# Performance work log

Hardware: AMD Instinct MI355X
Metric: run time of the kernel (lower is better)

The kernel has to match this reference:

```python
import jax, jax.numpy as jnp
import numpy as np

TOKENS, D_IN, D_OUT, R = 8192, 4096, 4096, 16
SCALE = 2.0

def setup_inputs() -> dict:
    key = jax.random.key(0)
    ks = jax.random.split(key, 5)
    return {
        "x": jax.random.normal(ks[0], (TOKENS, D_IN), dtype=jnp.float32),
        "weight": jax.random.normal(ks[1], (D_OUT, D_IN), dtype=jnp.float32) * 0.02,
        "bias": jax.random.normal(ks[2], (D_OUT,), dtype=jnp.float32) * 0.01,
        "lora_A": jax.random.normal(ks[3], (R, D_IN), dtype=jnp.float32) * 0.02,
        "lora_B": jax.random.normal(ks[4], (D_OUT, R), dtype=jnp.float32) * 0.02,
    }

def reference(x, weight, bias, lora_A, lora_B):
    # y = x W^T + bias + scale * x (B A)^T
    # Reassociate to avoid materializing the [D_OUT, D_IN] B@A matrix:
    # x (B A)^T = (x A^T) B^T  -- same math, low-rank path.
    base = jnp.einsum('ti,oi->to', x, weight) + bias          # [T, D_OUT]
    lora = jnp.einsum('tr,or->to', jnp.einsum('ti,ri->tr', x, lora_A), lora_B)
    return base + SCALE * lora
```

## Files before the change

kernel.cpp:

```cpp
#include <hip/hip_runtime.h>
#include <hip/hip_bf16.h>
#include <stdint.h>

#define TOKENS 8192
#define DIN 4096
#define DOUT 4096
#define RNK 16
#define LORA_SCALE 2.0f

typedef __attribute__((ext_vector_type(8))) __bf16 bf16x8;
typedef __attribute__((ext_vector_type(4))) float f32x4;

__device__ __forceinline__ unsigned short f2bf(float f) {
    union { float f; unsigned int u; } v; v.f = f;
    unsigned int u = v.u;
    unsigned int r = (u + 0x7fffu + ((u >> 16) & 1u)) >> 16;
    return (unsigned short)r;
}

__device__ __forceinline__ void async_copy16(const void* g, void* l) {
    __builtin_amdgcn_global_load_lds(
        (const __attribute__((address_space(1))) void*)g,
        (__attribute__((address_space(3))) void*)l,
        16, 0, 0);
}

__global__ void cast_x_kernel(const float4* __restrict__ x, ushort4* __restrict__ xb) {
    int i = blockIdx.x * blockDim.x + threadIdx.x;
    float4 v = x[i];
    ushort4 o;
    o.x = f2bf(v.x); o.y = f2bf(v.y); o.z = f2bf(v.z); o.w = f2bf(v.w);
    xb[i] = o;
}

__global__ void fold_w_kernel(const float* __restrict__ W,
                              const float* __restrict__ lA,
                              const float* __restrict__ lB,
                              ushort* __restrict__ Wb) {
    int o  = blockIdx.y;
    int i0 = (blockIdx.x * blockDim.x + threadIdx.x) * 4;
    __shared__ float sB[RNK];
    if (threadIdx.x < RNK) sB[threadIdx.x] = lB[(size_t)o * RNK + threadIdx.x];
    __syncthreads();
    float4 w = *(const float4*)(W + (size_t)o * DIN + i0);
    float ax = 0.f, ay = 0.f, az = 0.f, aw = 0.f;
#pragma unroll
    for (int r = 0; r < RNK; r++) {
        float4 a = *(const float4*)(lA + (size_t)r * DIN + i0);
        float b = sB[r];
        ax += b * a.x; ay += b * a.y; az += b * a.z; aw += b * a.w;
    }
    ushort4 outv;
    outv.x = f2bf(w.x + LORA_SCALE * ax);
    outv.y = f2bf(w.y + LORA_SCALE * ay);
    outv.z = f2bf(w.z + LORA_SCALE * az);
    outv.w = f2bf(w.w + LORA_SCALE * aw);
    *(ushort4*)(Wb + (size_t)o * DIN + i0) = outv;
}

#define BM 128
#define BN 128
#define BK 64

__global__ __launch_bounds__(256) void gemm_bias_kernel(
    const ushort* __restrict__ Xb, const ushort* __restrict__ Wb,
    const float* __restrict__ bias, float* __restrict__ Y) {
    const int N = DOUT, K = DIN;
    __shared__ ushort sA[BM * BK];
    __shared__ ushort sB[BN * BK];

    const int tid  = threadIdx.x;
    const int lane = tid & 63;
    const int wave = tid >> 6;
    const int m0 = blockIdx.y * BM;
    const int n0 = blockIdx.x * BN;

    const int wm64 = (wave & 1) * 64;
    const int wn64 = (wave >> 1) * 64;

    const int srow = tid >> 3;
    const int p    = tid & 7;
    const int scol = (p ^ (srow & 7)) * 8;
    const ushort* gA = Xb + (size_t)(m0 + srow) * K + scol;
    const ushort* gB = Wb + (size_t)(n0 + srow) * K + scol;
    ushort* lAp = &sA[tid * 8];
    ushort* lBp = &sB[tid * 8];

    const int lr  = lane & 15;
    const int q   = lane >> 4;
    const int swc = lr & 7;
    const int c0  = ((0 * 4 + q) ^ swc) * 8;
    const int c1  = ((1 * 4 + q) ^ swc) * 8;

    f32x4 acc[4][4] = {};

    for (int k0 = 0; k0 < K; k0 += BK) {
        __syncthreads();
#pragma unroll
        for (int j = 0; j < 4; j++) {
            async_copy16(gA + (size_t)(j * 32) * K, lAp + j * 2048);
            async_copy16(gB + (size_t)(j * 32) * K, lBp + j * 2048);
        }
        gA += BK; gB += BK;
        __syncthreads();

#pragma unroll
        for (int s = 0; s < 2; s++) {
            const int cs = s ? c1 : c0;
            bf16x8 af[4], bfr[4];
#pragma unroll
            for (int t = 0; t < 4; t++) {
                af[t]  = *(const bf16x8*)(&sA[(wm64 + t * 16 + lr) * BK + cs]);
                bfr[t] = *(const bf16x8*)(&sB[(wn64 + t * 16 + lr) * BK + cs]);
            }
#pragma unroll
            for (int im = 0; im < 4; im++)
#pragma unroll
                for (int in = 0; in < 4; in++)
                    acc[im][in] = __builtin_amdgcn_mfma_f32_16x16x32_bf16(
                        af[im], bfr[in], acc[im][in], 0, 0, 0);
        }
    }

    const int col  = lane & 15;
    const int qrow = (lane >> 4) * 4;
#pragma unroll
    for (int in = 0; in < 4; in++) {
        const int n = n0 + wn64 + in * 16 + col;
        const float bv = bias[n];
#pragma unroll
        for (int im = 0; im < 4; im++) {
            const int m = m0 + wm64 + im * 16 + qrow;
            float* yp = Y + (size_t)m * N + n;
            yp[0 * (size_t)N] = acc[im][in].x + bv;
            yp[1 * (size_t)N] = acc[im][in].y + bv;
            yp[2 * (size_t)N] = acc[im][in].z + bv;
            yp[3 * (size_t)N] = acc[im][in].w + bv;
        }
    }
}

extern "C" void kernel_launch(void* const* d_in, const int* in_sizes, int n_in,
                              void* d_out, int out_size, void* d_ws, size_t ws_size,
                              hipStream_t stream) {
    const float* x    = (const float*)d_in[0];
    const float* W    = (const float*)d_in[1];
    const float* bias = (const float*)d_in[2];
    const float* lA   = (const float*)d_in[3];
    const float* lB   = (const float*)d_in[4];
    float* Y = (float*)d_out;

    ushort* xb = (ushort*)d_ws;
    ushort* wb = xb + (size_t)TOKENS * DIN;

    cast_x_kernel<<<(TOKENS * DIN / 4) / 256, 256, 0, stream>>>(
        (const float4*)x, (ushort4*)xb);
    fold_w_kernel<<<dim3(DIN / (256 * 4), DOUT), 256, 0, stream>>>(W, lA, lB, wb);
    gemm_bias_kernel<<<dim3(DOUT / BN, TOKENS / BM), 256, 0, stream>>>(xb, wb, bias, Y);
}
```

Measured before the change: 605.8 us.

## Rewrite GEMM with 256x256 tiles, 4-stage async LDS pipeline and XCD swizzle

The bf16 GEMM moves to 256x256 block tiles with 512 threads, where each wave computes a 128x64 sub-tile. It adds a four-slot LDS ring fed by async global-to-LDS copies with explicit vmcnt waits, so loads run ahead while the MFMAs execute. It also remaps block IDs so neighbouring tiles land on the same XCD for better L2 reuse, and raises MFMA wave priority. In exchange it needs more registers per thread (128 accumulator floats) and 128 KB of LDS per block, and the correctness of the hand-written barrier and waitcnt schedule is a risk.

```diff
diff --git a/kernel.cpp b/kernel.cpp
--- a/kernel.cpp
+++ b/kernel.cpp
@@ -58,86 +58,134 @@
     *(ushort4*)(Wb + (size_t)o * DIN + i0) = outv;
 }
 
-#define BM 128
-#define BN 128
-#define BK 64
-
-__global__ __launch_bounds__(256) void gemm_bias_kernel(
+#define BM 256
+#define BN 256
+#define BK 32
+#define NTILES (DIN / BK)
+#define SLOT_U16 16384
+#define SLOT_BYTES 32768
+#define B_OFF_BYTES 16384
+
+__global__ __launch_bounds__(512, 2) void gemm_bias_kernel(
     const ushort* __restrict__ Xb, const ushort* __restrict__ Wb,
     const float* __restrict__ bias, float* __restrict__ Y) {
-    const int N = DOUT, K = DIN;
-    __shared__ ushort sA[BM * BK];
-    __shared__ ushort sB[BN * BK];
+
+    __shared__ ushort smem[4 * SLOT_U16];
 
     const int tid  = threadIdx.x;
     const int lane = tid & 63;
     const int wave = tid >> 6;
-    const int m0 = blockIdx.y * BM;
-    const int n0 = blockIdx.x * BN;
-
-    const int wm64 = (wave & 1) * 64;
-    const int wn64 = (wave >> 1) * 64;
-
-    const int srow = tid >> 3;
-    const int p    = tid & 7;
-    const int scol = (p ^ (srow & 7)) * 8;
-    const ushort* gA = Xb + (size_t)(m0 + srow) * K + scol;
-    const ushort* gB = Wb + (size_t)(n0 + srow) * K + scol;
-    ushort* lAp = &sA[tid * 8];
-    ushort* lBp = &sB[tid * 8];
-
-    const int lr  = lane & 15;
-    const int q   = lane >> 4;
-    const int swc = lr & 7;
-    const int c0  = ((0 * 4 + q) ^ swc) * 8;
-    const int c1  = ((1 * 4 + q) ^ swc) * 8;
-
-    f32x4 acc[4][4] = {};
-
-    for (int k0 = 0; k0 < K; k0 += BK) {
-        __syncthreads();
-#pragma unroll
-        for (int j = 0; j < 4; j++) {
-            async_copy16(gA + (size_t)(j * 32) * K, lAp + j * 2048);
-            async_copy16(gB + (size_t)(j * 32) * K, lBp + j * 2048);
-        }
-        gA += BK; gB += BK;
-        __syncthreads();
-
-#pragma unroll
-        for (int s = 0; s < 2; s++) {
-            const int cs = s ? c1 : c0;
-            bf16x8 af[4], bfr[4];
-#pragma unroll
-            for (int t = 0; t < 4; t++) {
-                af[t]  = *(const bf16x8*)(&sA[(wm64 + t * 16 + lr) * BK + cs]);
-                bfr[t] = *(const bf16x8*)(&sB[(wn64 + t * 16 + lr) * BK + cs]);
-            }
-#pragma unroll
-            for (int im = 0; im < 4; im++)
-#pragma unroll
-                for (int in = 0; in < 4; in++)
-                    acc[im][in] = __builtin_amdgcn_mfma_f32_16x16x32_bf16(
-                        af[im], bfr[in], acc[im][in], 0, 0, 0);
+
+    const int bid  = blockIdx.x;
+    const int sbid = (bid & 7) * 64 + (bid >> 3);
+    const int m0 = (sbid >> 4) * BM;
+    const int n0 = (sbid & 15) * BN;
+
+    const int wm = (wave >> 2) * 128;
+    const int wn = (wave & 3) * 64;
+
+    auto srcoff = [](int ci) -> size_t {
+        const int L = ci >> 3, p = ci & 7;
+        const int u = p ^ (L & 7);
+        return (size_t)(2 * L + (u >> 2)) * DIN + (size_t)((u & 3) * 8);
+    };
+    const ushort* pA0 = Xb + (size_t)m0 * DIN + srcoff(tid);
+    const ushort* pA1 = Xb + (size_t)m0 * DIN + srcoff(tid + 512);
+    const ushort* pB0 = Wb + (size_t)n0 * DIN + srcoff(tid);
+    const ushort* pB1 = Wb + (size_t)n0 * DIN + srcoff(tid + 512);
+
+#define STAGE_A(slot) do { \
+        ushort* d_ = smem + (slot) * SLOT_U16 + tid * 8; \
+        async_copy16(pA0, d_); async_copy16(pA1, d_ + 4096); \
+        pA0 += BK; pA1 += BK; } while (0)
+#define STAGE_B(slot) do { \
+        ushort* d_ = smem + (slot) * SLOT_U16 + 8192 + tid * 8; \
+        async_copy16(pB0, d_); async_copy16(pB1, d_ + 4096); \
+        pB0 += BK; pB1 += BK; } while (0)
+
+    const int lr = lane & 15, qq = lane >> 4;
+    const int pp = (qq + 4 * (lr & 1)) ^ ((lr >> 1) & 7);
+    const int offA = ((wm >> 1) + (lr >> 1)) * 128 + pp * 16;
+    const int offB = ((wn >> 1) + (lr >> 1)) * 128 + pp * 16;
+    const char* smemc = (const char*)smem;
+
+    f32x4 acc[8][4] = {};
+    bf16x8 af[4], bfr[4];
+
+    STAGE_A(0); STAGE_B(0);
+    STAGE_A(1); STAGE_B(1);
+    STAGE_A(2); STAGE_B(2);
+    asm volatile("s_waitcnt vmcnt(8)" ::: "memory");
+    __builtin_amdgcn_s_barrier();
+
+#pragma unroll 1
+    for (int t = 0; t < NTILES; ++t) {
+        const char* sa = smemc + (size_t)(t & 3) * SLOT_BYTES;
+        const char* sb = sa + B_OFF_BYTES;
+        const int  stslot  = (t + 3) & 3;
+        const bool doStage = (t + 3 < NTILES);
+
+#pragma unroll
+        for (int f = 0; f < 4; f++) af[f]  = *(const bf16x8*)(sa + offA + f * 1024);
+#pragma unroll
+        for (int f = 0; f < 4; f++) bfr[f] = *(const bf16x8*)(sb + offB + f * 1024);
+        if (doStage) STAGE_A(stslot);
+        __builtin_amdgcn_s_barrier();
+        asm volatile("s_waitcnt lgkmcnt(0)" ::: "memory");
+        __builtin_amdgcn_s_setprio(1);
+#pragma unroll
+        for (int mf = 0; mf < 4; mf++)
+#pragma unroll
+            for (int nf = 0; nf < 4; nf++)
+                acc[mf][nf] = __builtin_amdgcn_mfma_f32_16x16x32_bf16(
+                    af[mf], bfr[nf], acc[mf][nf], 0, 0, 0);
+        __builtin_amdgcn_s_setprio(0);
+        __builtin_amdgcn_s_barrier();
+
+#pragma unroll
+        for (int f = 0; f < 4; f++) af[f] = *(const bf16x8*)(sa + offA + (4 + f) * 1024);
+        if (doStage) STAGE_B(stslot);
+        __builtin_amdgcn_s_barrier();
+        asm volatile("s_waitcnt lgkmcnt(0)" ::: "memory");
+        __builtin_amdgcn_s_setprio(1);
+#pragma unroll
+        for (int mf = 0; mf < 4; mf++)
+#pragma unroll
+            for (int nf = 0; nf < 4; nf++)
+                acc[4 + mf][nf] = __builtin_amdgcn_mfma_f32_16x16x32_bf16(
+                    af[mf], bfr[nf], acc[4 + mf][nf], 0, 0, 0);
+        __builtin_amdgcn_s_setprio(0);
+
+        if (t + 3 < NTILES) {
+            asm volatile("s_waitcnt vmcnt(8)" ::: "memory");
+            __builtin_amdgcn_s_barrier();
+        } else if (t + 3 == NTILES) {
+            asm volatile("s_waitcnt vmcnt(4)" ::: "memory");
+            __builtin_amdgcn_s_barrier();
+        } else if (t + 2 == NTILES) {
+            asm volatile("s_waitcnt vmcnt(0)" ::: "memory");
+            __builtin_amdgcn_s_barrier();
         }
     }
 
     const int col  = lane & 15;
     const int qrow = (lane >> 4) * 4;
 #pragma unroll
-    for (int in = 0; in < 4; in++) {
-        const int n = n0 + wn64 + in * 16 + col;
+    for (int nf = 0; nf < 4; nf++) {
+        const int n = n0 + wn + nf * 16 + col;
         const float bv = bias[n];
 #pragma unroll
-        for (int im = 0; im < 4; im++) {
-            const int m = m0 + wm64 + im * 16 + qrow;
-            float* yp = Y + (size_t)m * N + n;
-            yp[0 * (size_t)N] = acc[im][in].x + bv;
-            yp[1 * (size_t)N] = acc[im][in].y + bv;
-            yp[2 * (size_t)N] = acc[im][in].z + bv;
-            yp[3 * (size_t)N] = acc[im][in].w + bv;
+        for (int mf = 0; mf < 8; mf++) {
+            const int m = m0 + wm + mf * 16 + qrow;
+            float* yp = Y + (size_t)m * DOUT + n;
+            yp[0]                  = acc[mf][nf].x + bv;
+            yp[(size_t)DOUT]       = acc[mf][nf].y + bv;
+            yp[2 * (size_t)DOUT]   = acc[mf][nf].z + bv;
+            yp[3 * (size_t)DOUT]   = acc[mf][nf].w + bv;
         }
     }
+#undef STAGE_A
+#undef STAGE_B
 }
 
 extern "C" void kernel_launch(void* const* d_in, const int* in_sizes, int n_in,
@@ -156,5 +204,6 @@
     cast_x_kernel<<<(TOKENS * DIN / 4) / 256, 256, 0, stream>>>(
         (const float4*)x, (ushort4*)xb);
     fold_w_kernel<<<dim3(DIN / (256 * 4), DOUT), 256, 0, stream>>>(W, lA, lB, wb);
-    gemm_bias_kernel<<<dim3(DOUT / BN, TOKENS / BM), 256, 0, stream>>>(xb, wb, bias, Y);
-}
+    gemm_bias_kernel<<<dim3((TOKENS / BM) * (DOUT / BN)), 512, 0, stream>>>(
+        xb, wb, bias, Y);
+}
```

Measured after the change: 550.1 us. 9.2% less time.

## Rewrite GEMM with 256x256 tiles, double-buffered async LDS pipeline, and block swizzle

Applied to the files above, without the earlier changes.

Replaces the 128x128 single-buffered GEMM with a 256x256 tile run by 512 threads (8 waves, each computing 128x64). The K loop keeps two LDS stages in flight, issuing async global-to-LDS copies for tile t+2 while MFMAs run on the current tile, and interleaves barriers, lgkmcnt/vmcnt waits and setprio to overlap loads with compute. Block IDs are remapped across groups of 8 to improve L2 reuse. The aim is to hide global latency and cut per-FLOP LDS traffic. In exchange it uses 128KB of LDS per block and more registers per thread, so fewer blocks fit per CU, and the barrier protocol is fragile.

```diff
diff --git a/kernel.cpp b/kernel.cpp
--- a/kernel.cpp
+++ b/kernel.cpp
@@ -58,86 +58,150 @@
     *(ushort4*)(Wb + (size_t)o * DIN + i0) = outv;
 }
 
-#define BM 128
-#define BN 128
+#define BM 256
+#define BN 256
 #define BK 64
-
-__global__ __launch_bounds__(256) void gemm_bias_kernel(
+#define NT (DIN / BK)
+#define AREG 0
+#define BREG 32768
+
+__global__ __launch_bounds__(512, 2) void gemm_bias_kernel(
     const ushort* __restrict__ Xb, const ushort* __restrict__ Wb,
     const float* __restrict__ bias, float* __restrict__ Y) {
-    const int N = DOUT, K = DIN;
-    __shared__ ushort sA[BM * BK];
-    __shared__ ushort sB[BN * BK];
+
+    __shared__ ushort smem[65536];
 
     const int tid  = threadIdx.x;
     const int lane = tid & 63;
     const int wave = tid >> 6;
-    const int m0 = blockIdx.y * BM;
-    const int n0 = blockIdx.x * BN;
-
-    const int wm64 = (wave & 1) * 64;
-    const int wn64 = (wave >> 1) * 64;
-
-    const int srow = tid >> 3;
-    const int p    = tid & 7;
-    const int scol = (p ^ (srow & 7)) * 8;
-    const ushort* gA = Xb + (size_t)(m0 + srow) * K + scol;
-    const ushort* gB = Wb + (size_t)(n0 + srow) * K + scol;
-    ushort* lAp = &sA[tid * 8];
-    ushort* lBp = &sB[tid * 8];
-
-    const int lr  = lane & 15;
-    const int q   = lane >> 4;
-    const int swc = lr & 7;
-    const int c0  = ((0 * 4 + q) ^ swc) * 8;
-    const int c1  = ((1 * 4 + q) ^ swc) * 8;
-
-    f32x4 acc[4][4] = {};
-
-    for (int k0 = 0; k0 < K; k0 += BK) {
-        __syncthreads();
-#pragma unroll
-        for (int j = 0; j < 4; j++) {
-            async_copy16(gA + (size_t)(j * 32) * K, lAp + j * 2048);
-            async_copy16(gB + (size_t)(j * 32) * K, lBp + j * 2048);
-        }
-        gA += BK; gB += BK;
-        __syncthreads();
-
-#pragma unroll
-        for (int s = 0; s < 2; s++) {
-            const int cs = s ? c1 : c0;
-            bf16x8 af[4], bfr[4];
-#pragma unroll
-            for (int t = 0; t < 4; t++) {
-                af[t]  = *(const bf16x8*)(&sA[(wm64 + t * 16 + lr) * BK + cs]);
-                bfr[t] = *(const bf16x8*)(&sB[(wn64 + t * 16 + lr) * BK + cs]);
-            }
-#pragma unroll
-            for (int im = 0; im < 4; im++)
-#pragma unroll
-                for (int in = 0; in < 4; in++)
-                    acc[im][in] = __builtin_amdgcn_mfma_f32_16x16x32_bf16(
-                        af[im], bfr[in], acc[im][in], 0, 0, 0);
-        }
+
+    const int bid  = blockIdx.x;
+    const int sbid = (bid & 7) * 64 + (bid >> 3);
+    const int m0 = (sbid >> 4) * BM;
+    const int n0 = (sbid & 15) * BN;
+
+    const int wm128 = (wave >> 2) * 128;
+    const int wn64  = (wave & 3) * 64;
+    const int hA  = wave >> 2;
+    const int hB  = wn64 >> 7;
+    const int nB0 = wn64 & 127;
+
+    const int rowL = tid >> 3;
+    const int uu   = (tid & 7) ^ (rowL & 7);
+    const size_t prebase = (size_t)rowL * DIN + (size_t)(uu * 8);
+    const ushort* pA = Xb + (size_t)m0 * DIN + prebase;
+    const ushort* pB = Wb + (size_t)n0 * DIN + prebase;
+
+#define STAGE_H(reg, src, h, t) do { \
+        ushort* d_ = smem + (reg) + ((((t) & 1) << 1) + (h)) * 8192 + tid * 8; \
+        const ushort* s_ = (src) + (size_t)(h) * (128 * (size_t)DIN) + (size_t)(t) * 64; \
+        async_copy16(s_, d_); \
+        async_copy16(s_ + (size_t)64 * DIN, d_ + 4096); \
+    } while (0)
+
+    const int lr = lane & 15, qq = lane >> 4;
+    const int l0 = lr * 128 + ((qq ^ (lr & 7)) * 16);
+    const int l1 = lr * 128 + (((4 + qq) ^ (lr & 7)) * 16);
+    const char* smemc = (const char*)smem;
+    const char* aS0 = smemc + (0 + hA) * 16384;
+    const char* aS1 = smemc + (2 + hA) * 16384;
+    const char* bS0 = smemc + 65536 + (0 + hB) * 16384 + nB0 * 128;
+    const char* bS1 = smemc + 65536 + (2 + hB) * 16384 + nB0 * 128;
+
+#define LD8(p) (*(const bf16x8*)(p))
+#define BAR_LGKM do { \
+        __builtin_amdgcn_s_barrier(); \
+        asm volatile("s_waitcnt lgkmcnt(0)" ::: "memory"); \
+        __builtin_amdgcn_sched_barrier(0); \
+        __builtin_amdgcn_s_setprio(1); \
+    } while (0)
+#define CLOSE do { \
+        __builtin_amdgcn_s_setprio(0); \
+        __builtin_amdgcn_s_barrier(); \
+    } while (0)
+#define MFMA_Q(mo, no, A_, B_) do { \
+        _Pragma("unroll") \
+        for (int m_ = 0; m_ < 4; m_++) \
+        _Pragma("unroll") \
+        for (int n_ = 0; n_ < 2; n_++) \
+        _Pragma("unroll") \
+        for (int k_ = 0; k_ < 2; k_++) \
+            acc[(mo) + m_][(no) + n_] = __builtin_amdgcn_mfma_f32_16x16x32_bf16( \
+                A_[m_][k_], B_[n_][k_], acc[(mo) + m_][(no) + n_], 0, 0, 0); \
+    } while (0)
+
+    f32x4 acc[8][4] = {};
+    bf16x8 aa[4][2], b0[2][2], b1[2][2];
+
+    STAGE_H(AREG, pA, 0, 0); STAGE_H(AREG, pA, 1, 0);
+    STAGE_H(BREG, pB, 0, 0); STAGE_H(BREG, pB, 1, 0);
+    STAGE_H(AREG, pA, 0, 1); STAGE_H(AREG, pA, 1, 1);
+    STAGE_H(BREG, pB, 0, 1); STAGE_H(BREG, pB, 1, 1);
+    asm volatile("s_waitcnt vmcnt(8)" ::: "memory");
+    __builtin_amdgcn_s_barrier();
+
+#define KTILE(AS, BS, ts, doSt) do { \
+         \
+        _Pragma("unroll") \
+        for (int m_ = 0; m_ < 4; m_++) { \
+            aa[m_][0] = LD8(AS + m_ * 2048 + l0); \
+            aa[m_][1] = LD8(AS + m_ * 2048 + l1); } \
+        _Pragma("unroll") \
+        for (int n_ = 0; n_ < 2; n_++) { \
+            b0[n_][0] = LD8(BS + n_ * 2048 + l0); \
+            b0[n_][1] = LD8(BS + n_ * 2048 + l1); } \
+        BAR_LGKM; MFMA_Q(0, 0, aa, b0); CLOSE; \
+         \
+        _Pragma("unroll") \
+        for (int n_ = 0; n_ < 2; n_++) { \
+            b1[n_][0] = LD8(BS + (n_ + 2) * 2048 + l0); \
+            b1[n_][1] = LD8(BS + (n_ + 2) * 2048 + l1); } \
+        BAR_LGKM; MFMA_Q(0, 2, aa, b1); CLOSE; \
+         \
+        _Pragma("unroll") \
+        for (int m_ = 0; m_ < 4; m_++) { \
+            aa[m_][0] = LD8(AS + (m_ + 4) * 2048 + l0); \
+            aa[m_][1] = LD8(AS + (m_ + 4) * 2048 + l1); } \
+        if (doSt) { STAGE_H(BREG, pB, 0, ts); STAGE_H(BREG, pB, 1, ts); } \
+        BAR_LGKM; MFMA_Q(4, 2, aa, b1); CLOSE; \
+         \
+        if (doSt) { STAGE_H(AREG, pA, 0, ts); STAGE_H(AREG, pA, 1, ts); } \
+        BAR_LGKM; MFMA_Q(4, 0, aa, b0); \
+        __builtin_amdgcn_s_setprio(0); \
+        if (doSt) { asm volatile("s_waitcnt vmcnt(8)" ::: "memory"); } \
+        else      { asm volatile("s_waitcnt vmcnt(0)" ::: "memory"); } \
+        __builtin_amdgcn_s_barrier(); \
+    } while (0)
+
+#pragma unroll 1
+    for (int it = 0; it < NT / 2; ++it) {
+        const int t0 = 2 * it, t1 = 2 * it + 1;
+        KTILE(aS0, bS0, t0 + 2, (t0 + 2 < NT));
+        KTILE(aS1, bS1, t1 + 2, (t1 + 2 < NT));
     }
 
     const int col  = lane & 15;
     const int qrow = (lane >> 4) * 4;
 #pragma unroll
-    for (int in = 0; in < 4; in++) {
-        const int n = n0 + wn64 + in * 16 + col;
+    for (int nf = 0; nf < 4; nf++) {
+        const int n = n0 + wn64 + nf * 16 + col;
         const float bv = bias[n];
 #pragma unroll
-        for (int im = 0; im < 4; im++) {
-            const int m = m0 + wm64 + im * 16 + qrow;
-            float* yp = Y + (size_t)m * N + n;
-            yp[0 * (size_t)N] = acc[im][in].x + bv;
-            yp[1 * (size_t)N] = acc[im][in].y + bv;
-            yp[2 * (size_t)N] = acc[im][in].z + bv;
-            yp[3 * (size_t)N] = acc[im][in].w + bv;
+        for (int mf = 0; mf < 8; mf++) {
+            const int m = m0 + wm128 + mf * 16 + qrow;
+            float* yp = Y + (size_t)m * DOUT + n;
+            yp[0]                = acc[mf][nf].x + bv;
+            yp[(size_t)DOUT]     = acc[mf][nf].y + bv;
+            yp[2 * (size_t)DOUT] = acc[mf][nf].z + bv;
+            yp[3 * (size_t)DOUT] = acc[mf][nf].w + bv;
         }
     }
+#undef STAGE_H
+#undef KTILE
+#undef MFMA_Q
+#undef BAR_LGKM
+#undef CLOSE
+#undef LD8
 }
 
 extern "C" void kernel_launch(void* const* d_in, const int* in_sizes, int n_in,
@@ -156,5 +220,6 @@
     cast_x_kernel<<<(TOKENS * DIN / 4) / 256, 256, 0, stream>>>(
         (const float4*)x, (ushort4*)xb);
     fold_w_kernel<<<dim3(DIN / (256 * 4), DOUT), 256, 0, stream>>>(W, lA, lB, wb);
-    gemm_bias_kernel<<<dim3(DOUT / BN, TOKENS / BM), 256, 0, stream>>>(xb, wb, bias, Y);
-}
+    gemm_bias_kernel<<<dim3((TOKENS / BM) * (DOUT / BN)), 512, 0, stream>>>(
+        xb, wb, bias, Y);
+}
```

New measurement: 535.4 us. 1.13x faster.

## Triple-buffer GEMM with 256x128 tiles, BK=32 and swizzled block order

Applied to the files above, without the earlier changes.

Restructures the bf16 GEMM to a 256x128 block tile with BK=32 and a three-slot LDS ring. Asynchronous global-to-LDS copies for tile t+2 are issued while tile t is computed, with vmcnt waits replacing the double __syncthreads per iteration. Block IDs are remapped so that groups of blocks share rows or columns for L2 reuse, and launch bounds request 2 blocks per CU. The cast kernel is also turned into a grid-stride loop with a fixed grid. Each wave now holds 8x4 accumulators, which raises register pressure.

```diff
diff --git a/kernel.cpp b/kernel.cpp
--- a/kernel.cpp
+++ b/kernel.cpp
@@ -26,11 +26,14 @@
 }
 
 __global__ void cast_x_kernel(const float4* __restrict__ x, ushort4* __restrict__ xb) {
-    int i = blockIdx.x * blockDim.x + threadIdx.x;
-    float4 v = x[i];
-    ushort4 o;
-    o.x = f2bf(v.x); o.y = f2bf(v.y); o.z = f2bf(v.z); o.w = f2bf(v.w);
-    xb[i] = o;
+    const int total = TOKENS * DIN / 4;
+    for (int i = blockIdx.x * blockDim.x + threadIdx.x; i < total;
+         i += gridDim.x * blockDim.x) {
+        float4 v = x[i];
+        ushort4 o;
+        o.x = f2bf(v.x); o.y = f2bf(v.y); o.z = f2bf(v.z); o.w = f2bf(v.w);
+        xb[i] = o;
+    }
 }
 
 __global__ void fold_w_kernel(const float* __restrict__ W,
@@ -58,86 +61,111 @@
     *(ushort4*)(Wb + (size_t)o * DIN + i0) = outv;
 }
 
-#define BM 128
+#define BM 256
 #define BN 128
-#define BK 64
+#define BK 32
+#define NT (DIN / BK)
+#define SLOT_U16 12288
+#define SLOT_BYTES 24576
+#define B_OFF_BYTES 16384
 
-__global__ __launch_bounds__(256) void gemm_bias_kernel(
+__global__ __launch_bounds__(256, 2) void gemm_bias_kernel(
     const ushort* __restrict__ Xb, const ushort* __restrict__ Wb,
     const float* __restrict__ bias, float* __restrict__ Y) {
-    const int N = DOUT, K = DIN;
-    __shared__ ushort sA[BM * BK];
-    __shared__ ushort sB[BN * BK];
+
+    __shared__ ushort smem[3 * SLOT_U16];
 
     const int tid  = threadIdx.x;
     const int lane = tid & 63;
     const int wave = tid >> 6;
-    const int m0 = blockIdx.y * BM;
-    const int n0 = blockIdx.x * BN;
 
-    const int wm64 = (wave & 1) * 64;
-    const int wn64 = (wave >> 1) * 64;
+    const int bid  = blockIdx.x;
+    const int sbid = (bid & 7) * 128 + (bid >> 3);
+    const int m0 = (sbid >> 5) * BM;
+    const int n0 = (sbid & 31) * BN;
 
-    const int srow = tid >> 3;
-    const int p    = tid & 7;
-    const int scol = (p ^ (srow & 7)) * 8;
-    const ushort* gA = Xb + (size_t)(m0 + srow) * K + scol;
-    const ushort* gB = Wb + (size_t)(n0 + srow) * K + scol;
-    ushort* lAp = &sA[tid * 8];
-    ushort* lBp = &sB[tid * 8];
+    const int wm = (wave >> 1) * 128;
+    const int wn = (wave & 1) * 64;
 
-    const int lr  = lane & 15;
-    const int q   = lane >> 4;
-    const int swc = lr & 7;
-    const int c0  = ((0 * 4 + q) ^ swc) * 8;
-    const int c1  = ((1 * 4 + q) ^ swc) * 8;
+    const int rowS = tid >> 2;
+    const int gS   = (tid & 3) ^ ((rowS >> 1) & 3);
+    const ushort* pA = Xb + (size_t)(m0 + rowS) * DIN + gS * 8;
+    const ushort* pB = Wb + (size_t)(n0 + rowS) * DIN + gS * 8;
 
-    f32x4 acc[4][4] = {};
+#define STAGE(slot, t_) do { \
+        const size_t ko_ = (size_t)(t_) * BK; \
+        ushort* dA_ = smem + (slot) * SLOT_U16 + tid * 8; \
+        const ushort* sA_ = pA + ko_; \
+        async_copy16(sA_,                    dA_); \
+        async_copy16(sA_ +  64 * (size_t)DIN, dA_ + 2048); \
+        async_copy16(sA_ + 128 * (size_t)DIN, dA_ + 4096); \
+        async_copy16(sA_ + 192 * (size_t)DIN, dA_ + 6144); \
+        ushort* dB_ = smem + (slot) * SLOT_U16 + 8192 + tid * 8; \
+        const ushort* sB_ = pB + ko_; \
+        async_copy16(sB_,                    dB_); \
+        async_copy16(sB_ +  64 * (size_t)DIN, dB_ + 2048); \
+    } while (0)
 
-    for (int k0 = 0; k0 < K; k0 += BK) {
-        __syncthreads();
+    const int lr = lane & 15, q = lane >> 4;
+    const int gF = q ^ ((lr >> 1) & 3);
+    const int offA = (wm + lr) * 64 + gF * 16;
+    const int offB = B_OFF_BYTES + (wn + lr) * 64 + gF * 16;
+    const char* smemc = (const char*)smem;
+
+    f32x4 acc[8][4] = {};
+
+    STAGE(0, 0);
+    STAGE(1, 1);
+    asm volatile("s_waitcnt vmcnt(6)" ::: "memory");
+    __builtin_amdgcn_s_barrier();
+
+    int s = 0, s2 = 2;
+#pragma unroll 1
+    for (int t = 0; t < NT; ++t) {
+        if (t + 2 < NT) STAGE(s2, t + 2);
+
+        const char* base = smemc + s * SLOT_BYTES;
+        bf16x8 af[8], bf[4];
 #pragma unroll
-        for (int j = 0; j < 4; j++) {
-            async_copy16(gA + (size_t)(j * 32) * K, lAp + j * 2048);
-            async_copy16(gB + (size_t)(j * 32) * K, lBp + j * 2048);
-        }
-        gA += BK; gB += BK;
-        __syncthreads();
+        for (int m = 0; m < 8; m++) af[m] = *(const bf16x8*)(base + offA + 1024 * m);
+#pragma unroll
+        for (int n = 0; n < 4; n++) bf[n] = *(const bf16x8*)(base + offB + 1024 * n);
 
 #pragma unroll
-        for (int s = 0; s < 2; s++) {
-            const int cs = s ? c1 : c0;
-            bf16x8 af[4], bfr[4];
+        for (int m = 0; m < 8; m++)
 #pragma unroll
-            for (int t = 0; t < 4; t++) {
-                af[t]  = *(const bf16x8*)(&sA[(wm64 + t * 16 + lr) * BK + cs]);
-                bfr[t] = *(const bf16x8*)(&sB[(wn64 + t * 16 + lr) * BK + cs]);
-            }
-#pragma unroll
-            for (int im = 0; im < 4; im++)
-#pragma unroll
-                for (int in = 0; in < 4; in++)
-                    acc[im][in] = __builtin_amdgcn_mfma_f32_16x16x32_bf16(
-                        af[im], bfr[in], acc[im][in], 0, 0, 0);
+            for (int n = 0; n < 4; n++)
+                acc[m][n] = __builtin_amdgcn_mfma_f32_16x16x32_bf16(
+                    af[m], bf[n], acc[m][n], 0, 0, 0);
+
+        if (t < NT - 2) {
+            asm volatile("s_waitcnt vmcnt(6)" ::: "memory");
+            __builtin_amdgcn_s_barrier();
+        } else if (t == NT - 2) {
+            asm volatile("s_waitcnt vmcnt(0)" ::: "memory");
+            __builtin_amdgcn_s_barrier();
         }
+        s  = (s  == 2) ? 0 : s  + 1;
+        s2 = (s2 == 2) ? 0 : s2 + 1;
     }
 
     const int col  = lane & 15;
     const int qrow = (lane >> 4) * 4;
 #pragma unroll
-    for (int in = 0; in < 4; in++) {
-        const int n = n0 + wn64 + in * 16 + col;
-        const float bv = bias[n];
+    for (int n = 0; n < 4; n++) {
+        const int nn = n0 + wn + n * 16 + col;
+        const float bv = bias[nn];
 #pragma unroll
-        for (int im = 0; im < 4; im++) {
-            const int m = m0 + wm64 + im * 16 + qrow;
-            float* yp = Y + (size_t)m * N + n;
-            yp[0 * (size_t)N] = acc[im][in].x + bv;
-            yp[1 * (size_t)N] = acc[im][in].y + bv;
-            yp[2 * (size_t)N] = acc[im][in].z + bv;
-            yp[3 * (size_t)N] = acc[im][in].w + bv;
+        for (int m = 0; m < 8; m++) {
+            const int mm = m0 + wm + m * 16 + qrow;
+            float* yp = Y + (size_t)mm * DOUT + nn;
+            yp[0]                = acc[m][n].x + bv;
+            yp[(size_t)DOUT]     = acc[m][n].y + bv;
+            yp[2 * (size_t)DOUT] = acc[m][n].z + bv;
+            yp[3 * (size_t)DOUT] = acc[m][n].w + bv;
         }
     }
+#undef STAGE
 }
 
 extern "C" void kernel_launch(void* const* d_in, const int* in_sizes, int n_in,
@@ -153,8 +181,8 @@
     ushort* xb = (ushort*)d_ws;
     ushort* wb = xb + (size_t)TOKENS * DIN;
 
-    cast_x_kernel<<<(TOKENS * DIN / 4) / 256, 256, 0, stream>>>(
-        (const float4*)x, (ushort4*)xb);
+    cast_x_kernel<<<2048, 256, 0, stream>>>((const float4*)x, (ushort4*)xb);
     fold_w_kernel<<<dim3(DIN / (256 * 4), DOUT), 256, 0, stream>>>(W, lA, lB, wb);
-    gemm_bias_kernel<<<dim3(DOUT / BN, TOKENS / BM), 256, 0, stream>>>(xb, wb, bias, Y);
+    gemm_bias_kernel<<<dim3((TOKENS / BM) * (DOUT / BN)), 256, 0, stream>>>(
+        xb, wb, bias, Y);
 }
```

After: 588.2 us. -2.9%, faster.
